# Optimization experiments

Measured on AMD Instinct MI355X. Metric: run time of the kernel, lower is better.

The kernel has to match this reference:

```python
import jax, jax.numpy as jnp
import numpy as np
from jax import lax

D_MODEL = 512
D_STATE = 16
D_CONV = 4
EXPAND = 2
D_INNER = EXPAND * D_MODEL
DT_RANK = (D_MODEL + 15) // 16  # ceil(d_model/16) = 32
B = 2
L = 2048


def _silu(x):
    return x * jax.nn.sigmoid(x)


def _mamba_block(x, norm_w, norm_b, in_w, conv_w, conv_b, xproj_w, dt_w, dt_b, A_log, D_skip, out_w):
    # x: [B, L, D_MODEL]; pre-norm residual Mamba block.
    Bsz = x.shape[0]
    mu = x.mean(-1, keepdims=True)
    xc0 = x - mu
    xn = xc0 * lax.rsqrt((xc0 * xc0).mean(-1, keepdims=True) + 1e-5)
    xn = xn * norm_w + norm_b
    # in_proj (no bias): [B, L, 2*D_INNER]
    xz = jnp.einsum('bld,ed->ble', xn, in_w)
    xc, z = jnp.split(xz, 2, axis=-1)
    # depthwise causal conv over time
    xt = xc.transpose(0, 2, 1)  # [B, D_INNER, L]
    xt = lax.conv_general_dilated(xt, conv_w[:, None, :], (1,), [(D_CONV - 1, 0)],
                                  feature_group_count=D_INNER,
                                  dimension_numbers=('NCH', 'OIH', 'NCH'))
    xc = _silu((xt + conv_b[None, :, None]).transpose(0, 2, 1))  # [B, L, D_INNER]
    # x_proj -> (dt, B, C)
    dbc = jnp.einsum('bld,ed->ble', xc, xproj_w)
    dt, Bs, Cs = jnp.split(dbc, [DT_RANK, DT_RANK + D_STATE], axis=-1)
    delta = jax.nn.softplus(jnp.einsum('blr,dr->bld', dt, dt_w) + dt_b)  # [B, L, D_INNER]
    A = -jnp.exp(A_log)  # [D_INNER, D_STATE]

    def step(h, inp):
        d_t, B_t, C_t, u_t = inp  # [B,d], [B,n], [B,n], [B,d]
        h = jnp.exp(d_t[..., None] * A) * h + (d_t * u_t)[..., None] * B_t[:, None, :]
        y_t = jnp.einsum('bdn,bn->bd', h, C_t)
        return h, y_t

    xs = (delta.transpose(1, 0, 2), Bs.transpose(1, 0, 2), Cs.transpose(1, 0, 2), xc.transpose(1, 0, 2))
    h0 = jnp.zeros((Bsz, D_INNER, D_STATE), x.dtype)
    _, ys = lax.scan(step, h0, xs)
    y = ys.transpose(1, 0, 2) + xc * D_skip  # skip connection D*u
    y = y * _silu(z)
    return x + jnp.einsum('ble,de->bld', y, out_w)


def setup_inputs() -> dict:
    key = jax.random.key(0)
    ks = jax.random.split(key, 12)
    f = lambda k, shape, s=0.02: jax.random.normal(k, shape, jnp.float32) * s
    return {
        'v': jax.random.normal(ks[0], (B, L, D_MODEL), jnp.float32),
        'a': jax.random.normal(ks[1], (B, L, D_MODEL), jnp.float32),
        't': jax.random.normal(ks[2], (B, L, D_MODEL), jnp.float32),
        'norm_w': jnp.ones((3, D_MODEL), jnp.float32),
        'norm_b': jnp.zeros((3, D_MODEL), jnp.float32),
        'in_w': f(ks[3], (3, 2 * D_INNER, D_MODEL)),
        'conv_w': f(ks[4], (3, D_INNER, D_CONV), 0.1),
        'conv_b': jnp.zeros((3, D_INNER), jnp.float32),
        'xproj_w': f(ks[5], (3, DT_RANK + 2 * D_STATE, D_INNER)),
        'dt_w': f(ks[6], (3, D_INNER, DT_RANK), 0.1),
        'dt_b': jnp.full((3, D_INNER), -4.6, jnp.float32),  # softplus(-4.6) ~ 0.01
        'A_log': jnp.tile(jnp.log(jnp.arange(1, D_STATE + 1, dtype=jnp.float32)), (3, D_INNER, 1)),
        'D_skip': jnp.ones((3, D_INNER), jnp.float32),
        'out_w': f(ks[7], (3, D_MODEL, D_INNER)),
        'couple_w': f(ks[8], (3, D_MODEL, D_MODEL)),
        'coef': jnp.full((3,), 0.1, jnp.float32),  # alpha, beta, gamma
    }


def reference(v, a, t, norm_w, norm_b, in_w, conv_w, conv_b, xproj_w, dt_w, dt_b, A_log, D_skip, out_w, couple_w, coef):
    # cross-modal residual injection
    v_in = v + coef[0] * jnp.einsum('bld,ed->ble', a, couple_w[0])
    a_in = a + coef[1] * jnp.einsum('bld,ed->ble', t, couple_w[1])
    t_in = t + coef[2] * jnp.einsum('bld,ed->ble', v, couple_w[2])
    x = jnp.stack([v_in, a_in, t_in])  # [3, B, L, D]
    outs = jax.vmap(_mamba_block)(x, norm_w, norm_b, in_w, conv_w, conv_b, xproj_w,
                                  dt_w, dt_b, A_log, D_skip, out_w)
    return (outs[0], outs[1], outs[2])
```

## Files before the change

### kernel.cpp

```cpp
#include <hip/hip_runtime.h>
#include <hip/hip_bf16.h>

#define MODS 3
#define BSZ 2
#define LSEQ 2048
#define DMODEL 512
#define DINNER 1024
#define DTRANK 32
#define NSTATE 16
#define DCONV 4
#define MROWS (BSZ*LSEQ)
#define NCHUNK 64
#define CHUNK 32

#define LOG2E 1.44269504088896f
#define LN2   0.69314718055995f

typedef __attribute__((ext_vector_type(8))) short short8v;
typedef __attribute__((ext_vector_type(4))) short short4v;
typedef __attribute__((ext_vector_type(2))) short short2v;
typedef __attribute__((ext_vector_type(4))) float f32x4;

#if __has_builtin(__builtin_amdgcn_exp2f)
#define EXP2F __builtin_amdgcn_exp2f
#else
#define EXP2F exp2f
#endif
#if __has_builtin(__builtin_amdgcn_rcpf)
#define RCPF __builtin_amdgcn_rcpf
#else
#define RCPF(x) (1.0f / (x))
#endif

__device__ __forceinline__ short f2bf(float x) {
    __hip_bfloat16 h = __float2bfloat16(x);
    return __builtin_bit_cast(short, h);
}
__device__ __forceinline__ float bf2f(short s) {
    return __uint_as_float(((unsigned)(unsigned short)s) << 16);
}
__device__ __forceinline__ void gl_lds16(const short* g, short* l) {
    __builtin_amdgcn_global_load_lds(
        (const __attribute__((address_space(1))) unsigned int*)g,
        (__attribute__((address_space(3))) unsigned int*)l, 16, 0, 0);
}
__device__ __forceinline__ float sigmoid_f(float x) {
    return RCPF(1.f + EXP2F(-x * LOG2E));
}

#define MFMAQ(QR)                                                                  \
    _Pragma("unroll")                                                              \
    for (int rf = 0; rf < 2; ++rf)                                                 \
        _Pragma("unroll")                                                          \
        for (int cf = 0; cf < 2; ++cf)                                             \
            _Pragma("unroll")                                                      \
            for (int kh = 0; kh < 2; ++kh)                                         \
                acc[QR][rf][cf] = __builtin_amdgcn_mfma_f32_16x16x32_bf16(         \
                    afr[rf][kh], bfr[cf][kh], acc[QR][rf][cf], 0, 0, 0);

__global__ __launch_bounds__(1024) void gemm8p_inproj(
    const __hip_bfloat16* __restrict__ A_, const __hip_bfloat16* __restrict__ B_,
    __hip_bfloat16* __restrict__ C_)
{
    constexpr int NT = 8;
    __shared__ alignas(16) short As[2 * 16384];
    __shared__ alignas(16) short Bs[2 * 8192];
    const int z = blockIdx.z;
    const int bm0 = blockIdx.x * 256;
    const int bn0 = blockIdx.y * 128;
    const short* Ag = (const short*)A_ + (long)z * 2097152 + (long)bm0 * 512;
    const short* Bg = (const short*)B_ + (long)z * 1048576 + (long)bn0 * 512;
    short* Cg = (short*)C_ + (long)z * 8388608;
    const int tid = threadIdx.x;
    const int lane = tid & 63;
    const int w = tid >> 6;
    const int wr = w >> 2;
    const int wc = w & 3;
    const int lr = lane & 15;
    const int sidx = lane >> 4;
    const int srow_l = tid >> 3;
    const int sgoff = ((tid & 7) ^ (srow_l & 7)) * 8;

    f32x4 acc[2][2][2];
    #pragma unroll
    for (int a = 0; a < 2; ++a)
        #pragma unroll
        for (int b = 0; b < 2; ++b)
            #pragma unroll
            for (int c = 0; c < 2; ++c)
                acc[a][b][c] = (f32x4){0.f, 0.f, 0.f, 0.f};

    short8v afr[2][2];
    short8v bfr[2][2];

    auto stageA = [&](int buf, int half, int t) {
        const int row = half * 128 + srow_l;
        gl_lds16(Ag + (long)row * 512 + t * 64 + sgoff,
                 As + buf * 16384 + half * 8192 + tid * 8);
    };
    auto stageB = [&](int buf, int t) {
        const int row = srow_l;
        gl_lds16(Bg + (long)row * 512 + t * 64 + sgoff,
                 Bs + buf * 8192 + tid * 8);
    };
    auto loadA = [&](int buf, int qr) {
        #pragma unroll
        for (int rf = 0; rf < 2; ++rf)
            #pragma unroll
            for (int kh = 0; kh < 2; ++kh) {
                const int ra = qr * 128 + wr * 32 + rf * 16 + lr;
                const int g = kh * 4 + sidx;
                afr[rf][kh] = *(const short8v*)&As[buf * 16384 + ra * 64 + ((g ^ (ra & 7)) << 3)];
            }
    };
    auto loadB = [&](int buf) {
        #pragma unroll
        for (int cf = 0; cf < 2; ++cf)
            #pragma unroll
            for (int kh = 0; kh < 2; ++kh) {
                const int rb = wc * 32 + cf * 16 + lr;
                const int g = kh * 4 + sidx;
                bfr[cf][kh] = *(const short8v*)&Bs[buf * 8192 + rb * 64 + ((g ^ (rb & 7)) << 3)];
            }
    };

    stageA(0, 0, 0); stageB(0, 0); stageA(0, 1, 0);

    for (int t = 0; t < NT; ++t) {
        const int p = t & 1;
        const bool stg = (t + 1) < NT;
        if (stg) { stageA(p ^ 1, 0, t + 1); stageB(p ^ 1, t + 1);
                   asm volatile("s_waitcnt vmcnt(3)" ::: "memory"); }
        else       asm volatile("s_waitcnt vmcnt(1)" ::: "memory");
        asm volatile("s_barrier" ::: "memory");
        loadA(p, 0); loadB(p);
        MFMAQ(0)
        asm volatile("s_barrier" ::: "memory");
        if (stg) { stageA(p ^ 1, 1, t + 1);
                   asm volatile("s_waitcnt vmcnt(3)" ::: "memory"); }
        else       asm volatile("s_waitcnt vmcnt(0)" ::: "memory");
        asm volatile("s_barrier" ::: "memory");
        loadA(p, 1);
        MFMAQ(1)
        asm volatile("s_barrier" ::: "memory");
    }

    #pragma unroll
    for (int qr = 0; qr < 2; ++qr)
        #pragma unroll
        for (int rf = 0; rf < 2; ++rf)
            #pragma unroll
            for (int r = 0; r < 4; ++r) {
                const int row = bm0 + qr * 128 + wr * 32 + rf * 16 + (lane >> 4) * 4 + r;
                #pragma unroll
                for (int cf = 0; cf < 2; ++cf) {
                    const int col = bn0 + wc * 32 + cf * 16 + lr;
                    Cg[(long)row * 2048 + col] = f2bf(acc[qr][rf][cf][r]);
                }
            }
}

template<int NT>
__global__ __launch_bounds__(1024) void gemm_p128(
    const __hip_bfloat16* __restrict__ A_, const __hip_bfloat16* __restrict__ B_,
    int lda, int ldb, long sA, long sB,
    float* __restrict__ Cf, __hip_bfloat16* __restrict__ Cb, int ldc, long sC,
    const float* __restrict__ res, const float* __restrict__ resB,
    const float* __restrict__ resC,
    const __hip_bfloat16* __restrict__ resbf, long sResb,
    const float* __restrict__ coef_base)
{
    __shared__ alignas(16) short As[2 * 8192];
    __shared__ alignas(16) short Bs[2 * 8192];
    const int z = blockIdx.z;
    const int bm0 = blockIdx.x * 128;
    const int bn0 = blockIdx.y * 128;
    const short* Ag = (const short*)A_ + (long)z * sA + (long)bm0 * lda;
    const short* Bg = (const short*)B_ + (long)z * sB + (long)bn0 * ldb;
    const int tid = threadIdx.x;
    const int lane = tid & 63;
    const int w = tid >> 6;
    const int wr = w >> 2;
    const int wc = w & 3;
    const int lr = lane & 15;
    const int sidx = lane >> 4;
    const int srow_l = tid >> 3;
    const int sgoff = ((tid & 7) ^ (srow_l & 7)) * 8;

    f32x4 acc[2][2];
    #pragma unroll
    for (int a = 0; a < 2; ++a)
        #pragma unroll
        for (int b = 0; b < 2; ++b)
            acc[a][b] = (f32x4){0.f, 0.f, 0.f, 0.f};

    short8v afr[2][2];
    short8v bfr[2][2];

    auto stageA = [&](int buf, int t) {
        gl_lds16(Ag + (long)srow_l * lda + t * 64 + sgoff, As + buf * 8192 + tid * 8);
    };
    auto stageB = [&](int buf, int t) {
        gl_lds16(Bg + (long)srow_l * ldb + t * 64 + sgoff, Bs + buf * 8192 + tid * 8);
    };
    auto loadAB = [&](int buf) {
        #pragma unroll
        for (int rf = 0; rf < 2; ++rf)
            #pragma unroll
            for (int kh = 0; kh < 2; ++kh) {
                const int ra = wr * 32 + rf * 16 + lr;
                const int g = kh * 4 + sidx;
                afr[rf][kh] = *(const short8v*)&As[buf * 8192 + ra * 64 + ((g ^ (ra & 7)) << 3)];
            }
        #pragma unroll
        for (int cf = 0; cf < 2; ++cf)
            #pragma unroll
            for (int kh = 0; kh < 2; ++kh) {
                const int rb = wc * 32 + cf * 16 + lr;
                const int g = kh * 4 + sidx;
                bfr[cf][kh] = *(const short8v*)&Bs[buf * 8192 + rb * 64 + ((g ^ (rb & 7)) << 3)];
            }
    };

    stageA(0, 0); stageB(0, 0);

    for (int t = 0; t < NT; ++t) {
        const int p = t & 1;
        const bool stg = (t + 1) < NT;
        if (stg) { stageA(p ^ 1, t + 1); stageB(p ^ 1, t + 1);
                   asm volatile("s_waitcnt vmcnt(2)" ::: "memory"); }
        else       asm volatile("s_waitcnt vmcnt(0)" ::: "memory");
        asm volatile("s_barrier" ::: "memory");
        loadAB(p);
        #pragma unroll
        for (int rf = 0; rf < 2; ++rf)
            #pragma unroll
            for (int cf = 0; cf < 2; ++cf)
                #pragma unroll
                for (int kh = 0; kh < 2; ++kh)
                    acc[rf][cf] = __builtin_amdgcn_mfma_f32_16x16x32_bf16(
                        afr[rf][kh], bfr[cf][kh], acc[rf][cf], 0, 0, 0);
        asm volatile("s_barrier" ::: "memory");
    }

    const float alpha = coef_base ? coef_base[z] : 1.0f;
    const float* resz = res ? ((z == 0) ? res : ((z == 1) ? resB : resC)) : nullptr;
    const short* resbz = resbf ? (const short*)resbf + (long)z * sResb : nullptr;
    float* Cfz = Cf ? Cf + (long)z * sC : nullptr;
    short* Cbz = Cb ? (short*)Cb + (long)z * sC : nullptr;
    #pragma unroll
    for (int rf = 0; rf < 2; ++rf)
        #pragma unroll
        for (int r = 0; r < 4; ++r) {
            const int row = bm0 + wr * 32 + rf * 16 + (lane >> 4) * 4 + r;
            #pragma unroll
            for (int cf = 0; cf < 2; ++cf) {
                const int col = bn0 + wc * 32 + cf * 16 + lr;
                float val = acc[rf][cf][r] * alpha;
                if (resz)  val += resz[(long)row * ldc + col];
                if (resbz) val += bf2f(resbz[(long)row * ldc + col]);
                if (Cfz) Cfz[(long)row * ldc + col] = val;
                else     Cbz[(long)row * ldc + col] = f2bf(val);
            }
        }
}

template<int NJ, int BK>
__global__ __launch_bounds__(256) void gemm_bf16(
    const __hip_bfloat16* __restrict__ A_, const __hip_bfloat16* __restrict__ B_,
    int K, int lda, int ldb, long sA, long sB,
    float* __restrict__ Cf, __hip_bfloat16* __restrict__ Cb, int ldc, long sC,
    const float* __restrict__ res, long sRes,
    const float* __restrict__ resB, const float* __restrict__ resC,
    const __hip_bfloat16* __restrict__ resbf, long sResb,
    const float* __restrict__ coef_base, int coef_stride,
    const float* __restrict__ bias, long sBias, int act)
{
    constexpr int BN = NJ * 32;
    constexpr int ASZ = 128 * BK;
    constexpr int BSZe = BN * BK;
    __shared__ alignas(16) short As[2 * ASZ];
    __shared__ alignas(16) short Bs[2 * BSZe];
    const int z = blockIdx.z;
    const int bm0 = blockIdx.x * 128;
    const int bn0 = blockIdx.y * BN;
    const short* Ag = (const short*)A_ + z * sA + (long)bm0 * lda;
    const short* Bg = (const short*)B_ + z * sB + (long)bn0 * ldb;
    const int tid = threadIdx.x;
    const int lane = tid & 63;
    const int w = tid >> 6;
    const int wr = w >> 1, wc = w & 1;
    const int lr = lane & 15;
    const int sidx = lane >> 4;

    constexpr int SLOTS = BK / 8;
    const int srow = tid / SLOTS;
    const int sslot = tid % SLOTS;
    int swz;
    if constexpr (BK == 64) swz = srow & 7;
    else                    swz = (srow >> 1) & 3;
    const int sgcol = (sslot ^ swz) * 8;
    int fA;
    if constexpr (BK == 64) fA = lr & 7;
    else                    fA = (lr >> 1) & 3;

    constexpr int AINSTR = ASZ / 2048;
    constexpr int BINSTR = BSZe / 2048;
    constexpr int RPI = 2048 / BK;

    f32x4 acc[4][NJ];
    #pragma unroll
    for (int i = 0; i < 4; ++i)
        #pragma unroll
        for (int j = 0; j < NJ; ++j)
            acc[i][j] = (f32x4){0.f, 0.f, 0.f, 0.f};

    auto stage = [&](int buf, int k0) {
        #pragma unroll
        for (int i = 0; i < AINSTR; ++i)
            gl_lds16(Ag + (long)(i * RPI + srow) * lda + k0 + sgcol,
                     As + buf * ASZ + i * 2048 + tid * 8);
        #pragma unroll
        for (int i = 0; i < BINSTR; ++i)
            gl_lds16(Bg + (long)(i * RPI + srow) * ldb + k0 + sgcol,
                     Bs + buf * BSZe + i * 2048 + tid * 8);
    };
    auto compute = [&](int buf) {
        #pragma unroll
        for (int kh = 0; kh < BK / 32; ++kh) {
            const int sl = ((kh * 4 + sidx) ^ fA) * 8;
            short8v af[4], bfr2[NJ];
            #pragma unroll
            for (int i = 0; i < 4; ++i)
                af[i] = *(const short8v*)&As[buf * ASZ + (wr * 64 + i * 16 + lr) * BK + sl];
            #pragma unroll
            for (int j = 0; j < NJ; ++j)
                bfr2[j] = *(const short8v*)&Bs[buf * BSZe + (wc * NJ * 16 + j * 16 + lr) * BK + sl];
            #pragma unroll
            for (int i = 0; i < 4; ++i)
                #pragma unroll
                for (int j = 0; j < NJ; ++j)
                    acc[i][j] = __builtin_amdgcn_mfma_f32_16x16x32_bf16(af[i], bfr2[j], acc[i][j], 0, 0, 0);
        }
    };

    stage(0, 0);
    __syncthreads();
    int cur = 0;
    for (int k0 = BK; k0 < K; k0 += BK) {
        stage(cur ^ 1, k0);
        compute(cur);
        __syncthreads();
        cur ^= 1;
    }
    compute(cur);

    const float alpha = coef_base ? coef_base[z * coef_stride] : 1.0f;
    const float* resz = nullptr;
    if (res) {
        if (resB) resz = (z == 0) ? res : ((z == 1) ? resB : resC);
        else      resz = res + z * sRes;
    }
    const short* resbz = resbf ? (const short*)resbf + (long)z * sResb : nullptr;
    const float* biasz = bias ? bias + z * sBias : nullptr;
    float* Cfz = Cf ? Cf + (long)z * sC : nullptr;
    __hip_bfloat16* Cbz = Cb ? Cb + (long)z * sC : nullptr;
    #pragma unroll
    for (int i = 0; i < 4; ++i) {
        #pragma unroll
        for (int r = 0; r < 4; ++r) {
            const int row = bm0 + wr * 64 + i * 16 + (lane >> 4) * 4 + r;
            #pragma unroll
            for (int j = 0; j < NJ; ++j) {
                const int col = bn0 + wc * NJ * 16 + j * 16 + lr;
                float val = acc[i][j][r];
                if (biasz) val += biasz[col];
                if (act == 1)
                    val = (val > 20.f) ? val : LN2 * __log2f(1.f + EXP2F(val * LOG2E));
                val *= alpha;
                if (resz)  val += resz[(long)row * ldc + col];
                if (resbz) val += bf2f(resbz[(long)row * ldc + col]);
                if (Cfz) Cfz[(long)row * ldc + col] = val;
                else     Cbz[(long)row * ldc + col] = __float2bfloat16(val);
            }
        }
    }
}

__global__ __launch_bounds__(256) void prep_kernel(
    const float* __restrict__ a, const float* __restrict__ t, const float* __restrict__ v,
    __hip_bfloat16* __restrict__ sec_bf,
    const float* __restrict__ couple_w, __hip_bfloat16* __restrict__ cw_bf,
    const float* __restrict__ in_w, __hip_bfloat16* __restrict__ inw_bf,
    const float* __restrict__ xproj_w, __hip_bfloat16* __restrict__ xpw_bf,
    const float* __restrict__ dt_w, __hip_bfloat16* __restrict__ dtw_bf,
    const float* __restrict__ out_w, __hip_bfloat16* __restrict__ outw_bf,
    const float* __restrict__ conv_w, float* __restrict__ cwT,
    const float* __restrict__ A_log, float* __restrict__ A2T)
{
    long idx = (long)blockIdx.x * 256 + threadIdx.x;
    if (idx < 1572864) {
        const int m = (int)(idx >> 19);
        const long off = idx & 524287;
        const float* sec = (m == 0) ? a : (m == 1) ? t : v;
        float4 sv = ((const float4*)sec)[off];
        short4v s;
        s.x = f2bf(sv.x); s.y = f2bf(sv.y); s.z = f2bf(sv.z); s.w = f2bf(sv.w);
        ((short4v*)sec_bf)[idx] = s;
        return;
    }
    idx -= 1572864;
    if (idx < 1449984) {
        const float* s; __hip_bfloat16* d; long off = idx;
        if      (off < 196608)              { s = couple_w; d = cw_bf; }
        else if ((off -= 196608) < 786432)  { s = in_w;     d = inw_bf; }
        else if ((off -= 786432) < 49152)   { s = xproj_w;  d = xpw_bf; }
        else if ((off -= 49152) < 24576)    { s = dt_w;     d = dtw_bf; }
        else    { off -= 24576;               s = out_w;    d = outw_bf; }
        float4 vv = ((const float4*)s)[off];
        short4v o;
        o.x = f2bf(vv.x); o.y = f2bf(vv.y); o.z = f2bf(vv.z); o.w = f2bf(vv.w);
        ((short4v*)d)[off] = o;
        return;
    }
    idx -= 1449984;
    if (idx < 12288) {
        const int k = (int)(idx & 3);
        const int c = (int)((idx >> 2) & 1023);
        const int m = (int)(idx >> 12);
        cwT[(m * DCONV + k) * DINNER + c] = conv_w[idx];
        return;
    }
    idx -= 12288;
    if (idx < 49152) {
        const int c = (int)(idx & 1023);
        const int n = (int)((idx >> 10) & 15);
        const int m = (int)(idx >> 14);
        A2T[idx] = -EXP2F(A_log[((long)m * DINNER + c) * NSTATE + n] * LOG2E) * LOG2E;
    }
}

__global__ __launch_bounds__(256) void ln_kernel(const __hip_bfloat16* __restrict__ x,
                                                 __hip_bfloat16* __restrict__ xn,
                                                 const float* __restrict__ nw, const float* __restrict__ nb)
{
    const int row = blockIdx.x;
    const int m = row >> 12;
    const int tid = threadIdx.x;
    const short2v vv = *(const short2v*)((const short*)x + (long)row * DMODEL + tid * 2);
    const float vx = bf2f(vv.x), vy = bf2f(vv.y);
    float s = vx + vy;
    float sq = vx * vx + vy * vy;
    #pragma unroll
    for (int off = 32; off > 0; off >>= 1) {
        s  += __shfl_down(s, off);
        sq += __shfl_down(sq, off);
    }
    __shared__ float ws_s[4], ws_q[4];
    const int wid = tid >> 6, lane = tid & 63;
    if (lane == 0) { ws_s[wid] = s; ws_q[wid] = sq; }
    __syncthreads();
    if (tid == 0) {
        float ts = ws_s[0] + ws_s[1] + ws_s[2] + ws_s[3];
        float tq = ws_q[0] + ws_q[1] + ws_q[2] + ws_q[3];
        float mu = ts / DMODEL;
        float var = tq / DMODEL - mu * mu;
        ws_s[0] = mu;
        ws_q[0] = rsqrtf(var + 1e-5f);
    }
    __syncthreads();
    const float mu = ws_s[0], rstd = ws_q[0];
    const int e0 = tid * 2;
    float2 w  = *reinterpret_cast<const float2*>(nw + m * DMODEL + e0);
    float2 bb = *reinterpret_cast<const float2*>(nb + m * DMODEL + e0);
    short2v o;
    o.x = f2bf((vx - mu) * rstd * w.x + bb.x);
    o.y = f2bf((vy - mu) * rstd * w.y + bb.y);
    *reinterpret_cast<short2v*>((short*)xn + (long)row * DMODEL + e0) = o;
}

__global__ __launch_bounds__(256) void conv_silu_kernel(const __hip_bfloat16* __restrict__ xz,
    const float* __restrict__ cwT, const float* __restrict__ cb, __hip_bfloat16* __restrict__ xc)
{
    const int idx = blockIdx.x * 256 + threadIdx.x;
    const int c8 = idx & 127;
    const int lt = (idx >> 7) & 255;
    const int mb = idx >> 15;
    const int m  = mb >> 1;
    const int c0 = c8 * 8;
    const int l0 = lt * 8;

    float4 wlo[DCONV], whi[DCONV];
    #pragma unroll
    for (int k = 0; k < DCONV; ++k) {
        wlo[k] = *(const float4*)&cwT[(m * DCONV + k) * DINNER + c0];
        whi[k] = *(const float4*)&cwT[(m * DCONV + k) * DINNER + c0 + 4];
    }
    const float4 blo = *(const float4*)&cb[m * DINNER + c0];
    const float4 bhi = *(const float4*)&cb[m * DINNER + c0 + 4];

    const short* base = (const short*)xz + (long)mb * LSEQ * 2048 + c0;
    short* obase = (short*)xc + (long)mb * LSEQ * DINNER + c0;

    short8v r0 = {}, r1 = {}, r2 = {};
    if (l0 - 3 >= 0) r0 = *(const short8v*)(base + (long)(l0 - 3) * 2048);
    if (l0 - 2 >= 0) r1 = *(const short8v*)(base + (long)(l0 - 2) * 2048);
    if (l0 - 1 >= 0) r2 = *(const short8v*)(base + (long)(l0 - 1) * 2048);

    #pragma unroll
    for (int i = 0; i < 8; ++i) {
        const short8v cur = *(const short8v*)(base + (long)(l0 + i) * 2048);
        float acc[8];
        #pragma unroll
        for (int j = 0; j < 4; ++j) {
            acc[j]     = ((const float*)&blo)[j];
            acc[4 + j] = ((const float*)&bhi)[j];
        }
        #pragma unroll
        for (int j = 0; j < 8; ++j) {
            const float w0 = (j < 4) ? ((const float*)&wlo[0])[j] : ((const float*)&whi[0])[j - 4];
            const float w1 = (j < 4) ? ((const float*)&wlo[1])[j] : ((const float*)&whi[1])[j - 4];
            const float w2 = (j < 4) ? ((const float*)&wlo[2])[j] : ((const float*)&whi[2])[j - 4];
            const float w3 = (j < 4) ? ((const float*)&wlo[3])[j] : ((const float*)&whi[3])[j - 4];
            acc[j] += w0 * bf2f(r0[j]) + w1 * bf2f(r1[j]) + w2 * bf2f(r2[j]) + w3 * bf2f(cur[j]);
        }
        short8v o;
        #pragma unroll
        for (int j = 0; j < 8; ++j)
            o[j] = f2bf(acc[j] * sigmoid_f(acc[j]));
        *(short8v*)(obase + (long)(l0 + i) * DINNER) = o;
        r0 = r1; r1 = r2; r2 = cur;
    }
}

__device__ __forceinline__ bool geo_check(const float* A2) {
    bool g = true;
    #pragma unroll
    for (int n = 1; n < NSTATE; ++n)
        g = g && (__builtin_fabsf(A2[n] - (float)(n + 1) * A2[0]) <= 1e-4f * __builtin_fabsf(A2[n]));
    return g;
}

__global__ __launch_bounds__(256) void scan_pass1_kernel(
    const __hip_bfloat16* __restrict__ delta, const __hip_bfloat16* __restrict__ xc,
    const __hip_bfloat16* __restrict__ dbc, const float* __restrict__ A2T,
    float* __restrict__ Fbuf, float* __restrict__ sumd)
{
    const int bx = blockIdx.x;
    const int chunk = bx & (NCHUNK - 1);
    const int cg = (bx >> 6) & 1;
    const int mb = bx >> 7;
    const int m = mb >> 1, b = mb & 1;
    const int tid = threadIdx.x;
    const int c0 = cg * 256 + tid;
    const int c1 = c0 + 512;

    float A2a[NSTATE], A2b[NSTATE];
    #pragma unroll
    for (int n = 0; n < NSTATE; ++n) {
        A2a[n] = A2T[((long)m * NSTATE + n) * DINNER + c0];
        A2b[n] = A2T[((long)m * NSTATE + n) * DINNER + c1];
    }
    const bool geo = geo_check(A2a) && geo_check(A2b);
    float h0[NSTATE] = {}, h1[NSTATE] = {};
    float sd0 = 0.f, sd1 = 0.f;

    __shared__ float sB[CHUNK][NSTATE];
    const short* dbc_mb = (const short*)dbc + (long)m * MROWS * 64 + (long)b * LSEQ * 64;
    const int t0 = chunk * CHUNK;
    for (int i = tid; i < CHUNK * NSTATE; i += 256) {
        int tt = i >> 4, j = i & 15;
        sB[tt][j] = bf2f(dbc_mb[(long)(t0 + tt) * 64 + 32 + j]);
    }
    __syncthreads();

    const short* dp = (const short*)delta;
    const short* up = (const short*)xc;
    const long base = ((long)mb * LSEQ + t0) * DINNER + c0;
    if (geo) {
        #pragma unroll 2
        for (int tt = 0; tt < CHUNK; ++tt) {
            const long ix = base + (long)tt * DINNER;
            const float d0 = bf2f(dp[ix]),       u0 = bf2f(up[ix]);
            const float d1 = bf2f(dp[ix + 512]), u1 = bf2f(up[ix + 512]);
            const float du0 = d0 * u0, du1 = d1 * u1;
            sd0 += d0; sd1 += d1;
            const float E0 = EXP2F(d0 * A2a[0]);
            const float E1 = EXP2F(d1 * A2b[0]);
            float e0 = 1.f, e1 = 1.f;
            #pragma unroll
            for (int n = 0; n < NSTATE; ++n) {
                e0 *= E0; e1 *= E1;
                h0[n] = e0 * h0[n] + du0 * sB[tt][n];
                h1[n] = e1 * h1[n] + du1 * sB[tt][n];
            }
        }
    } else {
        #pragma unroll 2
        for (int tt = 0; tt < CHUNK; ++tt) {
            const long ix = base + (long)tt * DINNER;
            const float d0 = bf2f(dp[ix]),       u0 = bf2f(up[ix]);
            const float d1 = bf2f(dp[ix + 512]), u1 = bf2f(up[ix + 512]);
            const float du0 = d0 * u0, du1 = d1 * u1;
            sd0 += d0; sd1 += d1;
            #pragma unroll
            for (int n = 0; n < NSTATE; ++n) {
                h0[n] = EXP2F(d0 * A2a[n]) * h0[n] + du0 * sB[tt][n];
                h1[n] = EXP2F(d1 * A2b[n]) * h1[n] + du1 * sB[tt][n];
            }
        }
    }
    const long ob = ((long)mb * NCHUNK + chunk) * (NSTATE * DINNER) + c0;
    #pragma unroll
    for (int n = 0; n < NSTATE; ++n) {
        Fbuf[ob + n * DINNER] = h0[n];
        Fbuf[ob + n * DINNER + 512] = h1[n];
    }
    const long so = (((long)mb * NCHUNK + chunk) << 10) + c0;
    sumd[so] = sd0;
    sumd[so + 512] = sd1;
}

__global__ __launch_bounds__(256) void scan_pass2_kernel(float* __restrict__ Fbuf,
                                                         const float* __restrict__ sumd,
                                                         const float* __restrict__ A2T)
{
    const long idx = (long)blockIdx.x * 256 + threadIdx.x;
    const int mb = (int)(idx >> 14);
    const int cn = (int)(idx & 16383);
    const int n = cn >> 10;
    const int c = cn & 1023;
    const int m = mb >> 1;
    const float A2n = A2T[((long)m * NSTATE + n) * DINNER + c];
    float run = 0.f;
    #pragma unroll 4
    for (int k = 0; k < NCHUNK; ++k) {
        const long o = ((long)(mb * NCHUNK + k) << 14) + cn;
        const float f = Fbuf[o];
        const float p = EXP2F(sumd[(((long)mb * NCHUNK + k) << 10) + c] * A2n);
        Fbuf[o] = run;
        run = p * run + f;
    }
}

__global__ __launch_bounds__(256) void scan_pass3_kernel(
    const __hip_bfloat16* __restrict__ delta, const __hip_bfloat16* __restrict__ xc,
    const __hip_bfloat16* __restrict__ dbc, __hip_bfloat16* __restrict__ xz,
    const float* __restrict__ A2T, const float* __restrict__ D_skip,
    const float* __restrict__ Hin)
{
    const int bx = blockIdx.x;
    const int chunk = bx & (NCHUNK - 1);
    const int cg = (bx >> 6) & 1;
    const int mb = bx >> 7;
    const int m = mb >> 1, b = mb & 1;
    const int tid = threadIdx.x;
    const int c0 = cg * 256 + tid;
    const int c1 = c0 + 512;

    float A2a[NSTATE], A2b[NSTATE];
    #pragma unroll
    for (int n = 0; n < NSTATE; ++n) {
        A2a[n] = A2T[((long)m * NSTATE + n) * DINNER + c0];
        A2b[n] = A2T[((long)m * NSTATE + n) * DINNER + c1];
    }
    const bool geo = geo_check(A2a) && geo_check(A2b);
    const float Dsk0 = D_skip[m * DINNER + c0];
    const float Dsk1 = D_skip[m * DINNER + c1];

    float h0[NSTATE], h1[NSTATE];
    const long ho = ((long)mb * NCHUNK + chunk) * (NSTATE * DINNER) + c0;
    #pragma unroll
    for (int n = 0; n < NSTATE; ++n) {
        h0[n] = Hin[ho + n * DINNER];
        h1[n] = Hin[ho + n * DINNER + 512];
    }

    __shared__ float sBC[CHUNK][2 * NSTATE];
    const short* dbc_mb = (const short*)dbc + (long)m * MROWS * 64 + (long)b * LSEQ * 64;
    const int t0 = chunk * CHUNK;
    for (int i = tid; i < CHUNK * 2 * NSTATE; i += 256) {
        int tt = i >> 5, j = i & 31;
        sBC[tt][j] = bf2f(dbc_mb[(long)(t0 + tt) * 64 + 32 + j]);
    }
    __syncthreads();

    const short* dp = (const short*)delta;
    const short* up = (const short*)xc;
    short* xzp = (short*)xz;
    const long base = ((long)mb * LSEQ + t0) * DINNER + c0;
    const long xbase = ((long)mb * LSEQ + t0) * 2048 + c0;
    if (geo) {
        #pragma unroll 2
        for (int tt = 0; tt < CHUNK; ++tt) {
            const long ix = base + (long)tt * DINNER;
            const long xi = xbase + (long)tt * 2048;
            const float d0 = bf2f(dp[ix]),       u0 = bf2f(up[ix]);
            const float d1 = bf2f(dp[ix + 512]), u1 = bf2f(up[ix + 512]);
            const float zv0 = bf2f(xzp[xi + 1024]);
            const float zv1 = bf2f(xzp[xi + 1536]);
            const float du0 = d0 * u0, du1 = d1 * u1;
            const float E0 = EXP2F(d0 * A2a[0]);
            const float E1 = EXP2F(d1 * A2b[0]);
            float e0 = 1.f, e1 = 1.f;
            float y0 = 0.f, y1 = 0.f;
            #pragma unroll
            for (int n = 0; n < NSTATE; ++n) {
                e0 *= E0; e1 *= E1;
                h0[n] = e0 * h0[n] + du0 * sBC[tt][n];
                h1[n] = e1 * h1[n] + du1 * sBC[tt][n];
                y0 += h0[n] * sBC[tt][16 + n];
                y1 += h1[n] * sBC[tt][16 + n];
            }
            y0 += u0 * Dsk0;
            y1 += u1 * Dsk1;
            xzp[xi]       = f2bf(y0 * (zv0 * sigmoid_f(zv0)));
            xzp[xi + 512] = f2bf(y1 * (zv1 * sigmoid_f(zv1)));
        }
    } else {
        #pragma unroll 2
        for (int tt = 0; tt < CHUNK; ++tt) {
            const long ix = base + (long)tt * DINNER;
            const long xi = xbase + (long)tt * 2048;
            const float d0 = bf2f(dp[ix]),       u0 = bf2f(up[ix]);
            const float d1 = bf2f(dp[ix + 512]), u1 = bf2f(up[ix + 512]);
            const float zv0 = bf2f(xzp[xi + 1024]);
            const float zv1 = bf2f(xzp[xi + 1536]);
            const float du0 = d0 * u0, du1 = d1 * u1;
            float y0 = 0.f, y1 = 0.f;
            #pragma unroll
            for (int n = 0; n < NSTATE; ++n) {
                h0[n] = EXP2F(d0 * A2a[n]) * h0[n] + du0 * sBC[tt][n];
                h1[n] = EXP2F(d1 * A2b[n]) * h1[n] + du1 * sBC[tt][n];
                y0 += h0[n] * sBC[tt][16 + n];
                y1 += h1[n] * sBC[tt][16 + n];
            }
            y0 += u0 * Dsk0;
            y1 += u1 * Dsk1;
            xzp[xi]       = f2bf(y0 * (zv0 * sigmoid_f(zv0)));
            xzp[xi + 512] = f2bf(y1 * (zv1 * sigmoid_f(zv1)));
        }
    }
}

extern "C" void kernel_launch(void* const* d_in, const int* in_sizes, int n_in,
                              void* d_out, int out_size, void* d_ws, size_t ws_size,
                              hipStream_t stream)
{
    const float* v       = (const float*)d_in[0];
    const float* a       = (const float*)d_in[1];
    const float* t       = (const float*)d_in[2];
    const float* norm_w  = (const float*)d_in[3];
    const float* norm_b  = (const float*)d_in[4];
    const float* in_w    = (const float*)d_in[5];
    const float* conv_w  = (const float*)d_in[6];
    const float* conv_b  = (const float*)d_in[7];
    const float* xproj_w = (const float*)d_in[8];
    const float* dt_w    = (const float*)d_in[9];
    const float* dt_b    = (const float*)d_in[10];
    const float* A_log   = (const float*)d_in[11];
    const float* D_skip  = (const float*)d_in[12];
    const float* out_w   = (const float*)d_in[13];
    const float* couple_w= (const float*)d_in[14];
    const float* coef    = (const float*)d_in[15];
    float* out = (float*)d_out;

    typedef __hip_bfloat16 bf;
    float* ws0    = (float*)d_ws;
    bf* x_in_bf   = (bf*)ws0;
    bf* xn_bf     = (bf*)(ws0 + 6291456);
    bf* sec_bf    = xn_bf + 6291456;
    bf* xz_bf     = sec_bf + 6291456;
    bf* xc_bf     = xz_bf + 25165824;
    bf* delta_bf  = xc_bf + 12582912;
    bf* dbc_bf    = delta_bf + 12582912;
    bf* cw_bf     = dbc_bf + 786432;
    bf* inw_bf    = cw_bf + 786432;
    bf* xpw_bf    = inw_bf + 3145728;
    bf* dtw_bf    = xpw_bf + 196608;
    bf* outw_bf   = dtw_bf + 98304;
    float* cwT    = (float*)(outw_bf + 1572864);
    float* A2T    = cwT + 12288;
    float* Fbuf   = A2T + 49152;
    float* sumd   = Fbuf + 6291456;

    dim3 blk(256);

    prep_kernel<<<(1572864 + 1449984 + 12288 + 49152 + 255) / 256, blk, 0, stream>>>(
        a, t, v, sec_bf, couple_w, cw_bf, in_w, inw_bf, xproj_w, xpw_bf,
        dt_w, dtw_bf, out_w, outw_bf, conv_w, cwT, A_log, A2T);

    gemm_p128<8><<<dim3(32, 4, 3), 1024, 0, stream>>>(
        sec_bf, cw_bf, 512, 512, 2097152L, 262144L,
        nullptr, x_in_bf, 512, 2097152L,
        v, a, t, nullptr, 0L, coef);
    ln_kernel<<<3*4096, blk, 0, stream>>>(x_in_bf, xn_bf, norm_w, norm_b);
    gemm8p_inproj<<<dim3(16, 16, 3), 1024, 0, stream>>>(xn_bf, inw_bf, xz_bf);
    conv_silu_kernel<<<768, blk, 0, stream>>>(xz_bf, cwT, conv_b, xc_bf);
    gemm_bf16<2, 64><<<dim3(32, 1, 3), blk, 0, stream>>>(
        xc_bf, xpw_bf, 1024, 1024, 1024, 4194304L, 65536L,
        nullptr, dbc_bf, 64, 262144L, nullptr, 0L, nullptr, nullptr, nullptr, 0L,
        nullptr, 0, nullptr, 0L, 0);
    gemm_bf16<4, 32><<<dim3(32, 8, 3), blk, 0, stream>>>(
        dbc_bf, dtw_bf, 32, 64, 32, 262144L, 32768L,
        nullptr, delta_bf, 1024, 4194304L, nullptr, 0L, nullptr, nullptr, nullptr, 0L,
        nullptr, 0, dt_b, 1024L, 1);
    scan_pass1_kernel<<<6*2*NCHUNK, blk, 0, stream>>>(delta_bf, xc_bf, dbc_bf, A2T, Fbuf, sumd);
    scan_pass2_kernel<<<(6*1024*16)/256, blk, 0, stream>>>(Fbuf, sumd, A2T);
    scan_pass3_kernel<<<6*2*NCHUNK, blk, 0, stream>>>(delta_bf, xc_bf, dbc_bf, xz_bf,
                                                      A2T, D_skip, Fbuf);
    gemm_p128<16><<<dim3(32, 4, 3), 1024, 0, stream>>>(
        xz_bf, outw_bf, 2048, 1024, 8388608L, 524288L,
        out, nullptr, 512, 2097152L,
        nullptr, nullptr, nullptr, x_in_bf, 2097152L, nullptr);
}
```

Measured before the change: 227.9 us.

## Halve scan chunk length and store inter-chunk states in bf16

Shrinks the chunked selective-scan chunk from 32 to 16 steps, doubling the number of chunks. This gives the per-chunk passes 1 and 3 twice as many blocks and halves their serial per-block work. To keep the chunk-state buffer the same size, the carried states are stored as bf16 instead of fp32, and block-index decoding now uses division by NCHUNK. In exchange, the pass-2 serial prefix over chunks gets twice as long, the sumd buffer doubles, and the bf16 rounding of carried states can reduce accuracy.

```diff
diff --git a/kernel.cpp b/kernel.cpp
--- a/kernel.cpp
+++ b/kernel.cpp
@@ -10,8 +10,8 @@
 #define NSTATE 16
 #define DCONV 4
 #define MROWS (BSZ*LSEQ)
-#define NCHUNK 64
-#define CHUNK 32
+#define NCHUNK 128
+#define CHUNK 16
 
 #define LOG2E 1.44269504088896f
 #define LN2   0.69314718055995f
@@ -544,12 +544,12 @@
 __global__ __launch_bounds__(256) void scan_pass1_kernel(
     const __hip_bfloat16* __restrict__ delta, const __hip_bfloat16* __restrict__ xc,
     const __hip_bfloat16* __restrict__ dbc, const float* __restrict__ A2T,
-    float* __restrict__ Fbuf, float* __restrict__ sumd)
+    __hip_bfloat16* __restrict__ Fbuf, float* __restrict__ sumd)
 {
     const int bx = blockIdx.x;
     const int chunk = bx & (NCHUNK - 1);
-    const int cg = (bx >> 6) & 1;
-    const int mb = bx >> 7;
+    const int cg = (bx / NCHUNK) & 1;
+    const int mb = bx / (2 * NCHUNK);
     const int m = mb >> 1, b = mb & 1;
     const int tid = threadIdx.x;
     const int c0 = cg * 256 + tid;
@@ -610,18 +610,19 @@
             }
         }
     }
+    short* Fp = (short*)Fbuf;
     const long ob = ((long)mb * NCHUNK + chunk) * (NSTATE * DINNER) + c0;
     #pragma unroll
     for (int n = 0; n < NSTATE; ++n) {
-        Fbuf[ob + n * DINNER] = h0[n];
-        Fbuf[ob + n * DINNER + 512] = h1[n];
+        Fp[ob + n * DINNER] = f2bf(h0[n]);
+        Fp[ob + n * DINNER + 512] = f2bf(h1[n]);
     }
     const long so = (((long)mb * NCHUNK + chunk) << 10) + c0;
     sumd[so] = sd0;
     sumd[so + 512] = sd1;
 }
 
-__global__ __launch_bounds__(256) void scan_pass2_kernel(float* __restrict__ Fbuf,
+__global__ __launch_bounds__(256) void scan_pass2_kernel(__hip_bfloat16* __restrict__ Fbuf,
                                                          const float* __restrict__ sumd,
                                                          const float* __restrict__ A2T)
 {
@@ -632,13 +633,14 @@
     const int c = cn & 1023;
     const int m = mb >> 1;
     const float A2n = A2T[((long)m * NSTATE + n) * DINNER + c];
+    short* Fp = (short*)Fbuf;
     float run = 0.f;
     #pragma unroll 4
     for (int k = 0; k < NCHUNK; ++k) {
         const long o = ((long)(mb * NCHUNK + k) << 14) + cn;
-        const float f = Fbuf[o];
+        const float f = bf2f(Fp[o]);
         const float p = EXP2F(sumd[(((long)mb * NCHUNK + k) << 10) + c] * A2n);
-        Fbuf[o] = run;
+        Fp[o] = f2bf(run);
         run = p * run + f;
     }
 }
@@ -647,12 +649,12 @@
     const __hip_bfloat16* __restrict__ delta, const __hip_bfloat16* __restrict__ xc,
     const __hip_bfloat16* __restrict__ dbc, __hip_bfloat16* __restrict__ xz,
     const float* __restrict__ A2T, const float* __restrict__ D_skip,
-    const float* __restrict__ Hin)
+    const __hip_bfloat16* __restrict__ Hin)
 {
     const int bx = blockIdx.x;
     const int chunk = bx & (NCHUNK - 1);
-    const int cg = (bx >> 6) & 1;
-    const int mb = bx >> 7;
+    const int cg = (bx / NCHUNK) & 1;
+    const int mb = bx / (2 * NCHUNK);
     const int m = mb >> 1, b = mb & 1;
     const int tid = threadIdx.x;
     const int c0 = cg * 256 + tid;
@@ -669,11 +671,12 @@
     const float Dsk1 = D_skip[m * DINNER + c1];
 
     float h0[NSTATE], h1[NSTATE];
+    const short* Hp = (const short*)Hin;
     const long ho = ((long)mb * NCHUNK + chunk) * (NSTATE * DINNER) + c0;
     #pragma unroll
     for (int n = 0; n < NSTATE; ++n) {
-        h0[n] = Hin[ho + n * DINNER];
-        h1[n] = Hin[ho + n * DINNER + 512];
+        h0[n] = bf2f(Hp[ho + n * DINNER]);
+        h1[n] = bf2f(Hp[ho + n * DINNER + 512]);
     }
 
     __shared__ float sBC[CHUNK][2 * NSTATE];
@@ -781,8 +784,8 @@
     bf* outw_bf   = dtw_bf + 98304;
     float* cwT    = (float*)(outw_bf + 1572864);
     float* A2T    = cwT + 12288;
-    float* Fbuf   = A2T + 49152;
-    float* sumd   = Fbuf + 6291456;
+    bf* Fbuf      = (bf*)(A2T + 49152);
+    float* sumd   = (float*)(Fbuf + 12582912);
 
     dim3 blk(256);
 
```

New measurement: 232.2 us. About the same (+1.9%).
